# Performance work log

Measured on AMD Instinct MI355X. Metric: run time of the kernel, lower is better.

## Reference

```python
import jax, jax.numpy as jnp
import numpy as np

B, T, H = 4, 2048, 512
HEADS = 8
D = H // HEADS  # head dim = 64


def setup_inputs() -> dict:
    key = jax.random.key(0)
    ks = jax.random.split(key, 5)
    s = 1.0 / np.sqrt(H)
    return {
        "x": jax.random.normal(ks[0], (B, T, H), dtype=jnp.float32),
        "w_qkv": jax.random.uniform(ks[1], (H, 3 * H), dtype=jnp.float32, minval=-s, maxval=s),
        "b_qkv": jax.random.uniform(ks[2], (3 * H,), dtype=jnp.float32, minval=-s, maxval=s),
        "w_proj": jax.random.uniform(ks[3], (H, H), dtype=jnp.float32, minval=-s, maxval=s),
        "b_proj": jax.random.uniform(ks[4], (H,), dtype=jnp.float32, minval=-s, maxval=s),
    }


def reference(x, w_qkv, b_qkv, w_proj, b_proj):
    b, t, h = x.shape
    scale = (h // HEADS) ** (-0.5)
    qkv = (x @ w_qkv + b_qkv).reshape(b, t, 3, HEADS, h // HEADS)
    q, k, v = qkv[:, :, 0], qkv[:, :, 1], qkv[:, :, 2]  # [b,t,heads,d]
    q = q * scale
    scores = jnp.einsum('bthd,bThd->bhtT', q, k)  # [b,heads,t,t]
    weights = jax.nn.softmax(scores, axis=-1)
    attn = jnp.einsum('bhtT,bThd->bthd', weights, v).reshape(b, t, h)
    return attn @ w_proj + b_proj
```

## Files before the change

kernel.cpp:

```cpp
#include <hip/hip_runtime.h>
#include <stdint.h>

typedef unsigned short u16;
typedef __attribute__((ext_vector_type(8))) __bf16 bf16x8;
typedef __attribute__((ext_vector_type(4))) __bf16 bf16x4;
typedef __attribute__((ext_vector_type(4))) float f32x4;
typedef __attribute__((ext_vector_type(2))) unsigned int u32x2;
typedef __attribute__((ext_vector_type(4))) unsigned int u32x4;

#define QSCALE 0.18033688011112042f

__device__ __forceinline__ u16 f2bf(float f) {
    uint32_t u = __builtin_bit_cast(uint32_t, f);
    u = (u + 0x7fffu + ((u >> 16) & 1u)) >> 16;
    return (u16)u;
}

__device__ __forceinline__ void gl_lds16(const u16* g, u16* l) {
    __builtin_amdgcn_global_load_lds(
        (__attribute__((address_space(1))) uint32_t*)(g),
        (__attribute__((address_space(3))) uint32_t*)(l), 16, 0, 0);
}

__global__ __launch_bounds__(256) void prep_k(const float* __restrict__ xf,
                                              u16* __restrict__ xbf,
                                              const float* __restrict__ wq,
                                              u16* __restrict__ wqkvT) {
    __shared__ u16 t[64][65];
    const int b = blockIdx.x;
    const int tid = threadIdx.x;
    if (b < 4096) {
        const size_t v = (size_t)b * 256 + tid;
        const f32x4 val = ((const f32x4*)xf)[v];
        u32x2 p;
        p.x = (uint32_t)f2bf(val.x) | ((uint32_t)f2bf(val.y) << 16);
        p.y = (uint32_t)f2bf(val.z) | ((uint32_t)f2bf(val.w) << 16);
        *(u32x2*)&xbf[v * 4] = p;
    } else {
        const int bb = b - 4096;
        const int bx = (bb % 24) << 6, by = (bb / 24) << 6;
        const int tx = tid & 63, ty = tid >> 6;
#pragma unroll
        for (int i = ty; i < 64; i += 4)
            t[i][tx] = f2bf(wq[(size_t)(by + i) * 1536 + bx + tx]);
        __syncthreads();
#pragma unroll
        for (int i = ty; i < 64; i += 4)
            wqkvT[(size_t)(bx + i) * 512 + by + tx] = t[tx][i];
    }
}

__global__ void transpose_cvt_k(const float* __restrict__ in,
                                u16* __restrict__ out, int R, int C) {
    __shared__ u16 t[64][65];
    const int bx = blockIdx.x << 6, by = blockIdx.y << 6;
    const int tx = threadIdx.x, ty = threadIdx.y;
#pragma unroll
    for (int i = ty; i < 64; i += 8)
        t[i][tx] = f2bf(in[(size_t)(by + i) * C + bx + tx]);
    __syncthreads();
#pragma unroll
    for (int i = ty; i < 64; i += 8) out[(size_t)(bx + i) * R + by + tx] = t[tx][i];
}

template <int EPI, int BN>
__global__ __launch_bounds__(256, 3) void gemm_bt_k(
    const u16* __restrict__ A, const u16* __restrict__ Bt,
    const float* __restrict__ bias,
    u16* __restrict__ Qb, u16* __restrict__ Kb, u16* __restrict__ Vt,
    float* __restrict__ OutF) {
    constexpr int MI = (BN == 128) ? 4 : 2;
    constexpr int SSTG = 2 * 128 * 32 + 2 * BN * 32;
    constexpr int SEPI = (EPI == 0) ? 128 * 136 : 0;
    constexpr int SMEM = SSTG > SEPI ? SSTG : SEPI;
    __shared__ u16 smem[SMEM];
    u16* lA = smem;
    u16* lB = smem + 2 * 128 * 32;

    const int tid = threadIdx.x;
    const int w = tid >> 6, l = tid & 63, quad = l >> 4, r = l & 15;
    const int tm = blockIdx.x << 7;
    const int tn = blockIdx.y * BN;
    const int wm = (BN == 128) ? ((w >> 1) << 6) : (w << 5);
    const int wn = (BN == 128) ? ((w & 1) << 6) : 0;
    const int srow = l >> 2, sch = (l & 3) << 3;

    f32x4 acc[MI][4];
#pragma unroll
    for (int i = 0; i < MI; ++i)
#pragma unroll
        for (int j = 0; j < 4; ++j) acc[i][j] = (f32x4){0.f, 0.f, 0.f, 0.f};

    auto stage = [&](int b, int kk) {
#pragma unroll
        for (int ii = 0; ii < 2; ++ii) {
            const int rowl = w * 32 + ii * 16;
            gl_lds16(A + (size_t)(tm + rowl + srow) * 512 + kk + sch,
                     &lA[b * 4096 + rowl * 32]);
        }
        if (BN == 128) {
#pragma unroll
            for (int ii = 0; ii < 2; ++ii) {
                const int rowl = w * 32 + ii * 16;
                gl_lds16(Bt + (size_t)(tn + rowl + srow) * 512 + kk + sch,
                         &lB[b * BN * 32 + rowl * 32]);
            }
        } else {
            const int rowl = w * 16;
            gl_lds16(Bt + (size_t)(tn + rowl + srow) * 512 + kk + sch,
                     &lB[b * BN * 32 + rowl * 32]);
        }
    };

    stage(0, 0);
    __syncthreads();

    int cur = 0;
    for (int kk = 0; kk < 512; kk += 32) {
        if (kk + 32 < 512) stage(cur ^ 1, kk + 32);
        bf16x8 af[MI], bfr[4];
#pragma unroll
        for (int mi = 0; mi < MI; ++mi)
            af[mi] =
                *(const bf16x8*)&lA[cur * 4096 + (wm + mi * 16 + r) * 32 + quad * 8];
#pragma unroll
        for (int ni = 0; ni < 4; ++ni)
            bfr[ni] =
                *(const bf16x8*)&lB[cur * BN * 32 + (wn + ni * 16 + r) * 32 + quad * 8];
#pragma unroll
        for (int mi = 0; mi < MI; ++mi)
#pragma unroll
            for (int ni = 0; ni < 4; ++ni)
                acc[mi][ni] = __builtin_amdgcn_mfma_f32_16x16x32_bf16(
                    af[mi], bfr[ni], acc[mi][ni], 0, 0, 0);
        __syncthreads();
        cur ^= 1;
    }

    if (EPI == 1) {
#pragma unroll
        for (int ni = 0; ni < 4; ++ni) {
            const int n = tn + wn + ni * 16 + r;
            const float bv = bias[n];
#pragma unroll
            for (int mi = 0; mi < MI; ++mi)
#pragma unroll
                for (int i = 0; i < 4; ++i) {
                    const int m = tm + wm + mi * 16 + quad * 4 + i;
                    OutF[(size_t)m * 512 + n] = acc[mi][ni][i] + bv;
                }
        }
    } else {
        const bool isV = (tn >= 1024);
        const bool isQ = (tn < 512);
#pragma unroll
        for (int ni = 0; ni < 4; ++ni) {
            const int nl = wn + ni * 16 + r;
            const float bv = bias[tn + nl];
#pragma unroll
            for (int mi = 0; mi < MI; ++mi)
#pragma unroll
                for (int i = 0; i < 4; ++i) {
                    const int ml = wm + mi * 16 + quad * 4 + i;
                    float v = acc[mi][ni][i] + bv;
                    if (isQ) v *= QSCALE;
                    const u16 hb = f2bf(v);
                    if (isV)
                        smem[nl * 136 + ml] = hb;
                    else
                        smem[ml * 136 + nl] = hb;
                }
        }
        __syncthreads();
        const int tbb = tm >> 11, tt = tm & 2047;
        if (!isV) {
            u16* base = isQ ? Qb : Kb;
            const int mlr = l >> 3, ls = l & 7;
#pragma unroll
            for (int rg = 0; rg < 4; ++rg)
#pragma unroll
                for (int h = 0; h < 2; ++h) {
                    const int ml = (w * 4 + rg) * 8 + mlr;
                    const int head = ((tn + h * 64) >> 6) & 7;
                    const int bh = tbb * 8 + head;
                    const u32x4 dv = *(const u32x4*)&smem[ml * 136 + h * 64 + ls * 8];
                    *(u32x4*)&base[((size_t)(bh * 2048 + tt + ml) << 6) + ls * 8] = dv;
                }
        } else {
            const int nlr = l >> 4, ls = l & 15;
#pragma unroll
            for (int j2 = 0; j2 < 8; ++j2) {
                const int nl = w * 32 + j2 * 4 + nlr;
                const int n = tn + nl;
                const int d = n & 63, head = (n >> 6) & 7;
                const int bh = tbb * 8 + head;
                const u32x4 dv = *(const u32x4*)&smem[nl * 136 + ls * 8];
                *(u32x4*)&Vt[((size_t)(bh * 64 + d) << 11) + tt + ls * 8] = dv;
            }
        }
    }
}

__global__ __launch_bounds__(256, 2) void attn_k(
    const u16* __restrict__ Qb, const u16* __restrict__ Kb,
    const u16* __restrict__ Vt, u16* __restrict__ attnb) {
    __shared__ u16 lk[3][64 * 64];
    __shared__ u16 lv[3][64 * 64];
    const int tid = threadIdx.x;
    const int w = tid >> 6, l = tid & 63, quad = l >> 4, r = l & 15;
    const int qt = blockIdx.x, bh = blockIdx.y;
    const size_t qbase = (size_t)bh * 2048 + qt * 128;
    const int srl = l >> 3;
    const int sg = (l & 7) ^ srl;

    const int rl = r & 7;
    const int rhi = r >> 3;
    const int skq = (r & 3) ^ (((r >> 2) & 1) << 1) ^ (((r >> 2) & 2) << 1);
    const int g0 = (quad ^ skq) << 3;

    bf16x8 qf[2][2];
#pragma unroll
    for (int qs = 0; qs < 2; ++qs)
#pragma unroll
        for (int hf = 0; hf < 2; ++hf)
            qf[qs][hf] = *(const bf16x8*)&Qb[((qbase + w * 32 + qs * 16 + r) << 6) +
                                            hf * 32 + quad * 8];

    const u32x4 onesu = {0x3F803F80u, 0x3F803F80u, 0x3F803F80u, 0x3F803F80u};
    const bf16x8 vones = __builtin_bit_cast(bf16x8, onesu);

    f32x4 o[2][4];
#pragma unroll
    for (int qs = 0; qs < 2; ++qs)
#pragma unroll
        for (int i = 0; i < 4; ++i) o[qs][i] = (f32x4){0.f, 0.f, 0.f, 0.f};
    f32x4 osum[2];
    osum[0] = (f32x4){0.f, 0.f, 0.f, 0.f};
    osum[1] = (f32x4){0.f, 0.f, 0.f, 0.f};

    auto stage = [&](int b, int kv0) {
#pragma unroll
        for (int ii = 0; ii < 2; ++ii) {
            const int chunk = w * 2 + ii;
            const int skr = (srl & 3) ^ ((chunk & 1) << 1) ^ ((chunk & 2) << 1);
            gl_lds16(Kb + ((size_t)(bh * 2048 + kv0 + chunk * 8 + srl) << 6) +
                         ((l & 7) ^ skr) * 8,
                     &lk[b][chunk * 512]);
            gl_lds16(Vt + (((size_t)(bh * 64 + chunk * 8 + srl)) << 11) + kv0 + sg * 8,
                     &lv[b][chunk * 512]);
        }
    };

    int Roff[4];
#pragma unroll
    for (int kt = 0; kt < 4; ++kt) {
        const int R = (kt & 1) * 32 + (r >> 2) * 8 + (kt >> 1) * 4 + (r & 3);
        Roff[kt] = R * 64 + g0;
    }

    auto readK = [&](int b, bf16x8 (&ka)[4], bf16x8 (&kb)[4]) {
        const u16* base = &lk[b][0];
#pragma unroll
        for (int kt = 0; kt < 4; ++kt) {
            ka[kt] = *(const bf16x8*)&base[Roff[kt]];
            kb[kt] = *(const bf16x8*)&base[Roff[kt] ^ 32];
        }
    };

    stage(0, 0);
    stage(1, 64);
    __syncthreads();

    bf16x8 kaE[4], kbE[4], kaO[4], kbO[4];
    readK(0, kaE, kbE);

    int cur = 0, nx1 = 1, nx2 = 2;

    auto body = [&](int t, bf16x8 (&kaP)[4], bf16x8 (&kbP)[4],
                    bf16x8 (&kaN)[4], bf16x8 (&kbN)[4]) {
        if (t + 2 < 32) stage(nx2, (t + 2) * 64);
        bf16x8 vb[2][4];
#pragma unroll
        for (int h = 0; h < 2; ++h)
#pragma unroll
            for (int dt = 0; dt < 4; ++dt) {
                const int baseV = (dt * 2 + rhi) * 512 + rl * 64;
                vb[h][dt] = *(const bf16x8*)&lv[cur][baseV + ((h * 4 + quad) ^ rl) * 8];
            }
        bf16x4 pk4[2][4];
#pragma unroll
        for (int kt = 0; kt < 4; ++kt) {
#pragma unroll
            for (int qs = 0; qs < 2; ++qs) {
                f32x4 z = (f32x4){0.f, 0.f, 0.f, 0.f};
                __builtin_amdgcn_s_setprio(1);
                z = __builtin_amdgcn_mfma_f32_16x16x32_bf16(kaP[kt], qf[qs][0], z, 0, 0, 0);
                z = __builtin_amdgcn_mfma_f32_16x16x32_bf16(kbP[kt], qf[qs][1], z, 0, 0, 0);
                __builtin_amdgcn_s_setprio(0);
                bf16x4 pb;
                pb[0] = (__bf16)__builtin_amdgcn_exp2f(z[0]);
                pb[1] = (__bf16)__builtin_amdgcn_exp2f(z[1]);
                pb[2] = (__bf16)__builtin_amdgcn_exp2f(z[2]);
                pb[3] = (__bf16)__builtin_amdgcn_exp2f(z[3]);
                pk4[qs][kt] = pb;
            }
        }
        if (t + 1 < 32) readK(nx1, kaN, kbN);
        __builtin_amdgcn_s_setprio(1);
#pragma unroll
        for (int h = 0; h < 2; ++h) {
            const bf16x8 ap0 = __builtin_shufflevector(pk4[0][h], pk4[0][h + 2],
                                                       0, 1, 2, 3, 4, 5, 6, 7);
            const bf16x8 ap1 = __builtin_shufflevector(pk4[1][h], pk4[1][h + 2],
                                                       0, 1, 2, 3, 4, 5, 6, 7);
#pragma unroll
            for (int dt = 0; dt < 4; ++dt) {
                o[0][dt] = __builtin_amdgcn_mfma_f32_16x16x32_bf16(ap0, vb[h][dt],
                                                                  o[0][dt], 0, 0, 0);
                o[1][dt] = __builtin_amdgcn_mfma_f32_16x16x32_bf16(ap1, vb[h][dt],
                                                                  o[1][dt], 0, 0, 0);
            }
            osum[0] = __builtin_amdgcn_mfma_f32_16x16x32_bf16(ap0, vones, osum[0], 0, 0, 0);
            osum[1] = __builtin_amdgcn_mfma_f32_16x16x32_bf16(ap1, vones, osum[1], 0, 0, 0);
        }
        __builtin_amdgcn_s_setprio(0);

        __syncthreads();
        const int tmp = cur;
        cur = nx1;
        nx1 = nx2;
        nx2 = tmp;
    };

    for (int t = 0; t < 32; t += 2) {
        body(t, kaE, kbE, kaO, kbO);
        body(t + 1, kaO, kbO, kaE, kbE);
    }

    const int bb = bh >> 3, head = bh & 7;
#pragma unroll
    for (int qs = 0; qs < 2; ++qs) {
#pragma unroll
        for (int i = 0; i < 4; ++i) {
            const float inv = __builtin_amdgcn_rcpf(osum[qs][i]);
            const int row = bb * 2048 + qt * 128 + w * 32 + qs * 16 + quad * 4 + i;
#pragma unroll
            for (int dt = 0; dt < 4; ++dt)
                attnb[(size_t)row * 512 + head * 64 + dt * 16 + r] =
                    f2bf(o[qs][dt][i] * inv);
        }
    }
}

extern "C" void kernel_launch(void* const* d_in, const int* in_sizes, int n_in,
                              void* d_out, int out_size, void* d_ws, size_t ws_size,
                              hipStream_t stream) {
    const float *x = nullptr, *wq = nullptr, *bq = nullptr, *wp = nullptr, *bp = nullptr;
    for (int i = 0; i < n_in; ++i) {
        switch (in_sizes[i]) {
            case 4194304: x  = (const float*)d_in[i]; break;
            case 786432:  wq = (const float*)d_in[i]; break;
            case 1536:    bq = (const float*)d_in[i]; break;
            case 262144:  wp = (const float*)d_in[i]; break;
            case 512:     bp = (const float*)d_in[i]; break;
        }
    }
    if (!x || !wq || !bq || !wp || !bp) {
        x = (const float*)d_in[0]; wq = (const float*)d_in[1];
        bq = (const float*)d_in[2]; wp = (const float*)d_in[3];
        bp = (const float*)d_in[4];
    }
    float* out = (float*)d_out;

    char* ws = (char*)d_ws;
    u16* attnb  = (u16*)(ws + 0);
    u16* wqkvT  = (u16*)(ws + 0);
    u16* Qb     = (u16*)(ws + 8388608);
    u16* wprojT = (u16*)(ws + 8388608);
    u16* Kb     = (u16*)(ws + 16777216);
    u16* Vt     = (u16*)(ws + 25165824);
    u16* xbf    = (u16*)d_out;

    prep_k<<<dim3(4288), 256, 0, stream>>>(x, xbf, wq, wqkvT);
    gemm_bt_k<0, 128><<<dim3(64, 12), 256, 0, stream>>>(xbf, wqkvT, bq, Qb, Kb, Vt,
                                                        nullptr);
    attn_k<<<dim3(16, 32), 256, 0, stream>>>(Qb, Kb, Vt, attnb);
    transpose_cvt_k<<<dim3(8, 8), dim3(64, 8), 0, stream>>>(wp, wprojT, 512, 512);
    gemm_bt_k<1, 64><<<dim3(64, 8), 256, 0, stream>>>(attnb, wprojT, bp, nullptr,
                                                      nullptr, nullptr, out);
}
```

Measured before the change: 153.3 us.

## Deepen LDS prefetch pipelines with counted vmcnt waits instead of full syncs

```diff
diff --git a/kernel.cpp b/kernel.cpp
--- a/kernel.cpp
+++ b/kernel.cpp
@@ -20,6 +20,22 @@
     __builtin_amdgcn_global_load_lds(
         (__attribute__((address_space(1))) uint32_t*)(g),
         (__attribute__((address_space(3))) uint32_t*)(l), 16, 0, 0);
+}
+
+__device__ __forceinline__ void cbar4() {
+    asm volatile("s_waitcnt vmcnt(4)" ::: "memory");
+    __builtin_amdgcn_s_barrier();
+    __builtin_amdgcn_sched_barrier(0);
+}
+__device__ __forceinline__ void cbar3() {
+    asm volatile("s_waitcnt vmcnt(3)" ::: "memory");
+    __builtin_amdgcn_s_barrier();
+    __builtin_amdgcn_sched_barrier(0);
+}
+__device__ __forceinline__ void cbar0() {
+    asm volatile("s_waitcnt vmcnt(0)" ::: "memory");
+    __builtin_amdgcn_s_barrier();
+    __builtin_amdgcn_sched_barrier(0);
 }
 
 __global__ __launch_bounds__(256) void prep_k(const float* __restrict__ xf,
@@ -70,12 +86,12 @@
     u16* __restrict__ Qb, u16* __restrict__ Kb, u16* __restrict__ Vt,
     float* __restrict__ OutF) {
     constexpr int MI = (BN == 128) ? 4 : 2;
-    constexpr int SSTG = 2 * 128 * 32 + 2 * BN * 32;
+    constexpr int SSTG = 3 * 128 * 32 + 3 * BN * 32;
     constexpr int SEPI = (EPI == 0) ? 128 * 136 : 0;
     constexpr int SMEM = SSTG > SEPI ? SSTG : SEPI;
     __shared__ u16 smem[SMEM];
     u16* lA = smem;
-    u16* lB = smem + 2 * 128 * 32;
+    u16* lB = smem + 3 * 128 * 32;
 
     const int tid = threadIdx.x;
     const int w = tid >> 6, l = tid & 63, quad = l >> 4, r = l & 15;
@@ -113,11 +129,16 @@
     };
 
     stage(0, 0);
-    __syncthreads();
-
-    int cur = 0;
+    stage(1, 32);
+
+    int cur = 0, nx1 = 1, nx2 = 2;
     for (int kk = 0; kk < 512; kk += 32) {
-        if (kk + 32 < 512) stage(cur ^ 1, kk + 32);
+        if (kk < 480) {
+            if (BN == 128) cbar4(); else cbar3();
+        } else {
+            cbar0();
+        }
+        if (kk + 64 < 512) stage(nx2, kk + 64);
         bf16x8 af[MI], bfr[4];
 #pragma unroll
         for (int mi = 0; mi < MI; ++mi)
@@ -133,8 +154,7 @@
             for (int ni = 0; ni < 4; ++ni)
                 acc[mi][ni] = __builtin_amdgcn_mfma_f32_16x16x32_bf16(
                     af[mi], bfr[ni], acc[mi][ni], 0, 0, 0);
-        __syncthreads();
-        cur ^= 1;
+        const int tmp = cur; cur = nx1; nx1 = nx2; nx2 = tmp;
     }
 
     if (EPI == 1) {
@@ -151,6 +171,7 @@
                 }
         }
     } else {
+        __syncthreads();
         const bool isV = (tn >= 1024);
         const bool isQ = (tn < 512);
 #pragma unroll
@@ -204,8 +225,8 @@
 __global__ __launch_bounds__(256, 2) void attn_k(
     const u16* __restrict__ Qb, const u16* __restrict__ Kb,
     const u16* __restrict__ Vt, u16* __restrict__ attnb) {
-    __shared__ u16 lk[3][64 * 64];
-    __shared__ u16 lv[3][64 * 64];
+    __shared__ u16 lk[4][64 * 64];
+    __shared__ u16 lv[4][64 * 64];
     const int tid = threadIdx.x;
     const int w = tid >> 6, l = tid & 63, quad = l >> 4, r = l & 15;
     const int qt = blockIdx.x, bh = blockIdx.y;
@@ -269,16 +290,19 @@
 
     stage(0, 0);
     stage(1, 64);
-    __syncthreads();
-
+    stage(2, 128);
+    cbar4();
     bf16x8 kaE[4], kbE[4], kaO[4], kbO[4];
     readK(0, kaE, kbE);
 
-    int cur = 0, nx1 = 1, nx2 = 2;
+    int cur = 0, nx1 = 1, nx2 = 2, nx3 = 3;
 
     auto body = [&](int t, bf16x8 (&kaP)[4], bf16x8 (&kbP)[4],
                     bf16x8 (&kaN)[4], bf16x8 (&kbN)[4]) {
-        if (t + 2 < 32) stage(nx2, (t + 2) * 64);
+        if (t > 0) {
+            if (t < 30) cbar4(); else cbar0();
+        }
+        if (t + 3 < 32) stage(nx3, (t + 3) * 64);
         bf16x8 vb[2][4];
 #pragma unroll
         for (int h = 0; h < 2; ++h)
@@ -325,11 +349,7 @@
         }
         __builtin_amdgcn_s_setprio(0);
 
-        __syncthreads();
-        const int tmp = cur;
-        cur = nx1;
-        nx1 = nx2;
-        nx2 = tmp;
+        const int tmp = cur; cur = nx1; nx1 = nx2; nx2 = nx3; nx3 = tmp;
     };
 
     for (int t = 0; t < 32; t += 2) {
```

Result: no change. 155.2 us (+1.2%).

## Fold w_proj transpose into prep kernel and remap attention blocks per XCD

Applied to the files above, without the earlier changes.

```diff
diff --git a/kernel.cpp b/kernel.cpp
--- a/kernel.cpp
+++ b/kernel.cpp
@@ -25,7 +25,9 @@
 __global__ __launch_bounds__(256) void prep_k(const float* __restrict__ xf,
                                               u16* __restrict__ xbf,
                                               const float* __restrict__ wq,
-                                              u16* __restrict__ wqkvT) {
+                                              u16* __restrict__ wqkvT,
+                                              const float* __restrict__ wp,
+                                              u16* __restrict__ wprojT) {
     __shared__ u16 t[64][65];
     const int b = blockIdx.x;
     const int tid = threadIdx.x;
@@ -37,30 +39,22 @@
         p.y = (uint32_t)f2bf(val.z) | ((uint32_t)f2bf(val.w) << 16);
         *(u32x2*)&xbf[v * 4] = p;
     } else {
-        const int bb = b - 4096;
-        const int bx = (bb % 24) << 6, by = (bb / 24) << 6;
+        const bool isWq = (b < 4288);
+        const int bb = isWq ? (b - 4096) : (b - 4288);
+        const int nbx = isWq ? 24 : 8;
+        const int C = isWq ? 1536 : 512;
+        const float* src = isWq ? wq : wp;
+        u16* dst = isWq ? wqkvT : wprojT;
+        const int bx = (bb % nbx) << 6, by = (bb / nbx) << 6;
         const int tx = tid & 63, ty = tid >> 6;
 #pragma unroll
         for (int i = ty; i < 64; i += 4)
-            t[i][tx] = f2bf(wq[(size_t)(by + i) * 1536 + bx + tx]);
+            t[i][tx] = f2bf(src[(size_t)(by + i) * C + bx + tx]);
         __syncthreads();
 #pragma unroll
         for (int i = ty; i < 64; i += 4)
-            wqkvT[(size_t)(bx + i) * 512 + by + tx] = t[tx][i];
-    }
-}
-
-__global__ void transpose_cvt_k(const float* __restrict__ in,
-                                u16* __restrict__ out, int R, int C) {
-    __shared__ u16 t[64][65];
-    const int bx = blockIdx.x << 6, by = blockIdx.y << 6;
-    const int tx = threadIdx.x, ty = threadIdx.y;
-#pragma unroll
-    for (int i = ty; i < 64; i += 8)
-        t[i][tx] = f2bf(in[(size_t)(by + i) * C + bx + tx]);
-    __syncthreads();
-#pragma unroll
-    for (int i = ty; i < 64; i += 8) out[(size_t)(bx + i) * R + by + tx] = t[tx][i];
+            dst[(size_t)(bx + i) * 512 + by + tx] = t[tx][i];
+    }
 }
 
 template <int EPI, int BN>
@@ -208,7 +202,10 @@
     __shared__ u16 lv[3][64 * 64];
     const int tid = threadIdx.x;
     const int w = tid >> 6, l = tid & 63, quad = l >> 4, r = l & 15;
-    const int qt = blockIdx.x, bh = blockIdx.y;
+    const int bid = blockIdx.x + 16 * blockIdx.y;
+    const int xcd = bid & 7, idx = bid >> 3;
+    const int bh = xcd * 4 + (idx >> 4);
+    const int qt = idx & 15;
     const size_t qbase = (size_t)bh * 2048 + qt * 128;
     const int srl = l >> 3;
     const int sg = (l & 7) ^ srl;
@@ -376,16 +373,15 @@
     u16* attnb  = (u16*)(ws + 0);
     u16* wqkvT  = (u16*)(ws + 0);
     u16* Qb     = (u16*)(ws + 8388608);
-    u16* wprojT = (u16*)(ws + 8388608);
     u16* Kb     = (u16*)(ws + 16777216);
     u16* Vt     = (u16*)(ws + 25165824);
+    u16* wprojT = (u16*)(ws + 33554432);
     u16* xbf    = (u16*)d_out;
 
-    prep_k<<<dim3(4288), 256, 0, stream>>>(x, xbf, wq, wqkvT);
+    prep_k<<<dim3(4352), 256, 0, stream>>>(x, xbf, wq, wqkvT, wp, wprojT);
     gemm_bt_k<0, 128><<<dim3(64, 12), 256, 0, stream>>>(xbf, wqkvT, bq, Qb, Kb, Vt,
                                                         nullptr);
     attn_k<<<dim3(16, 32), 256, 0, stream>>>(Qb, Kb, Vt, attnb);
-    transpose_cvt_k<<<dim3(8, 8), dim3(64, 8), 0, stream>>>(wp, wprojT, 512, 512);
     gemm_bt_k<1, 64><<<dim3(64, 8), 256, 0, stream>>>(attnb, wprojT, bp, nullptr,
                                                       nullptr, nullptr, out);
 }
```

Result: no change. 151.3 us (-1.3%).
